# Optimization experiments

Hardware: AMD Instinct MI355X
Metric: run time of the kernel (lower is better)

The kernel has to match this reference:

```python
import jax, jax.numpy as jnp
import numpy as np

N_NODES = 100000

def setup_inputs() -> dict:
    key = jax.random.key(0)
    k1, k2, k3, k4, k5 = jax.random.split(key, 5)
    F_in, H, C = 128, 64, 40
    x = jax.random.normal(k1, (N_NODES, F_in), dtype=jnp.float32)
    edge_index = jax.random.randint(k2, (2, 1600000), 0, N_NODES, dtype=jnp.int64)
    # GCNConv weights (no bias), Glorot-ish scale
    W0 = jax.random.normal(k3, (F_in, H), dtype=jnp.float32) / np.sqrt(F_in)
    W1 = jax.random.normal(k4, (H, H), dtype=jnp.float32) / np.sqrt(H)
    W2 = jax.random.normal(k5, (H, C), dtype=jnp.float32) / np.sqrt(H)
    return {"x": x, "edge_index": edge_index, "W0": W0, "W1": W1, "W2": W2}


def _gcn_norm(edge_index, num_nodes):
    # Add self-loops, compute symmetric normalization D^-1/2 A D^-1/2
    loop = jnp.arange(num_nodes, dtype=edge_index.dtype)
    src = jnp.concatenate([edge_index[0], loop])
    dst = jnp.concatenate([edge_index[1], loop])
    deg = jax.ops.segment_sum(jnp.ones_like(dst, dtype=jnp.float32), dst,
                              num_segments=num_nodes)
    dinv = jnp.where(deg > 0, jax.lax.rsqrt(deg), 0.0)
    norm = dinv[src] * dinv[dst]  # [E + N]
    return src, dst, norm


def reference(x, edge_index, W0, W1, W2):
    N = x.shape[0]
    src, dst, norm = _gcn_norm(edge_index, N)

    def conv(h, W):
        h = h @ W                                   # [N, d_out]
        msg = h[src] * norm[:, None]                # gather + scale  [E+N, d_out]
        return jax.ops.segment_sum(msg, dst, num_segments=N)

    h = jax.nn.relu(conv(x, W0))
    h = jax.nn.relu(conv(h, W1))
    h = jax.nn.relu(conv(h, W2))
    return h
```

## Files before the change

### kernel.cpp

```cpp
#include <hip/hip_runtime.h>
#include <hip/hip_fp16.h>

#define N_FEAT0 128
#define HID 64
#define NCLS 40

#define BSH 9
#define BSZ 512
#define BCAP 12288
#define STILE 16384

__global__ __launch_bounds__(256) void scatter_kernel(const int* __restrict__ esrc,
                                                      const int* __restrict__ edst,
                                                      int* __restrict__ bfill,
                                                      int* __restrict__ slab, int E) {
  __shared__ int cnt[256];
  __shared__ int base[256];
  int t = threadIdx.x;
  int t0 = blockIdx.x * STILE;
  cnt[t] = 0;
  __syncthreads();

#pragma unroll 4
  for (int i = 0; i < STILE / 1024; ++i) {
    int e = t0 + i * 1024 + t * 4;
    if (e < E) {
      int4 d4 = *(const int4*)(edst + e);
      atomicAdd(&cnt[d4.x >> BSH], 1);
      atomicAdd(&cnt[d4.y >> BSH], 1);
      atomicAdd(&cnt[d4.z >> BSH], 1);
      atomicAdd(&cnt[d4.w >> BSH], 1);
    }
  }
  __syncthreads();
  int c = cnt[t];
  if (c > 0) base[t] = t * BCAP + atomicAdd(&bfill[t], c);
  cnt[t] = 0;
  __syncthreads();

#pragma unroll 4
  for (int i = 0; i < STILE / 1024; ++i) {
    int e = t0 + i * 1024 + t * 4;
    if (e < E) {
      int4 s4 = *(const int4*)(esrc + e);
      int4 d4 = *(const int4*)(edst + e);
#define EMIT(dd, ss)                                             \
      {                                                          \
        int b_ = (dd) >> BSH;                                    \
        int r_ = atomicAdd(&cnt[b_], 1);                         \
        slab[base[b_] + r_] = (((dd) & (BSZ - 1)) << 17) | (ss); \
      }
      EMIT(d4.x, s4.x)
      EMIT(d4.y, s4.y)
      EMIT(d4.z, s4.z)
      EMIT(d4.w, s4.w)
#undef EMIT
    }
  }
}

__global__ __launch_bounds__(256) void build_kernel(const int* __restrict__ slab,
                                                    const int* __restrict__ bfill,
                                                    int* __restrict__ row_ptr,
                                                    float* __restrict__ dinv,
                                                    int* __restrict__ ew,
                                                    int N, int nbuck) {
  __shared__ int cnt[512];
  __shared__ int pre[512];
  __shared__ int s2[256];
  int b = blockIdx.x;
  int t = threadIdx.x;
  int nbase = b << BSH;
  int nNodes = N - nbase;
  if (nNodes > BSZ) nNodes = BSZ;

  s2[t] = (t < nbuck) ? bfill[t] : 0;
  __syncthreads();
  for (int off = 1; off < 256; off <<= 1) {
    int u = (t >= off) ? s2[t - off] : 0;
    __syncthreads();
    s2[t] += u;
    __syncthreads();
  }
  int sz = bfill[b];
  int obase = s2[b] - sz;
  if (b == 0 && t == 255) row_ptr[N] = s2[255];
  __syncthreads();

  cnt[t] = 0;
  cnt[t + 256] = 0;
  __syncthreads();

  int sbeg = b * BCAP;

  for (int r = t; r < sz; r += 256) atomicAdd(&cnt[((unsigned)slab[sbeg + r]) >> 17], 1);
  __syncthreads();

  int a = cnt[2 * t], c = cnt[2 * t + 1];
  s2[t] = a + c;
  __syncthreads();
  for (int off = 1; off < 256; off <<= 1) {
    int u = (t >= off) ? s2[t - off] : 0;
    __syncthreads();
    s2[t] += u;
    __syncthreads();
  }
  int ex = s2[t] - (a + c);
  pre[2 * t] = ex;
  pre[2 * t + 1] = ex + a;
  __syncthreads();

  if (t < nNodes) {
    row_ptr[nbase + t] = obase + pre[t];
    dinv[nbase + t] = rsqrtf((float)(cnt[t] + 1));
  }
  int t2 = t + 256;
  if (t2 < nNodes) {
    row_ptr[nbase + t2] = obase + pre[t2];
    dinv[nbase + t2] = rsqrtf((float)(cnt[t2] + 1));
  }
  __syncthreads();
  cnt[t] = 0;
  cnt[t + 256] = 0;
  __syncthreads();

  for (int r = t; r < sz; r += 256) {
    int rec = slab[sbeg + r];
    int dloc = ((unsigned)rec) >> 17;
    int rank = atomicAdd(&cnt[dloc], 1);
    ew[obase + pre[dloc] + rank] = rec & 0x1FFFF;
  }
}

template <int K, int NC>
__global__ __launch_bounds__(256) void gemm_kernel(const float* __restrict__ A,
                                                   const float* __restrict__ W,
                                                   __half* __restrict__ Out,
                                                   const float* __restrict__ rowscale,
                                                   int N) {
  constexpr int BK = 64;
  constexpr int LDSS = 68;
  __shared__ float As[128 * LDSS];

  int t = threadIdx.x;
  int lane = t & 63;
  int wave = t >> 6;
  int c4 = lane & 15;
  int qr = lane >> 4;
  int r0 = blockIdx.x * 128;

  int wc = 4 * c4;
  if (wc > NC - 4) wc = NC - 4;
  bool cok = (wc == 4 * c4);

  float4 acc[8];
#pragma unroll
  for (int m = 0; m < 8; ++m) acc[m] = make_float4(0.f, 0.f, 0.f, 0.f);

  for (int kc = 0; kc < K; kc += BK) {
    __syncthreads();
#pragma unroll
    for (int i = 0; i < 8; ++i) {
      int idx = t + i * 256;
      int row = idx >> 4;
      int cq = idx & 15;
      int gr = r0 + row;
      if (gr >= N) gr = N - 1;
      float4 v = *(const float4*)(A + (size_t)gr * K + kc + 4 * cq);
      *(float4*)(As + row * LDSS + 4 * cq) = v;
    }
    __syncthreads();

#pragma unroll 2
    for (int kk = 0; kk < BK / 4; ++kk) {
      float4 w[4];
#pragma unroll
      for (int k = 0; k < 4; ++k)
        w[k] = *(const float4*)(W + (size_t)(kc + kk * 4 + k) * NC + wc);
#pragma unroll
      for (int m = 0; m < 8; ++m) {
        int lrow = wave * 32 + qr + 4 * m;
        float4 a = *(const float4*)(As + lrow * LDSS + kk * 4);
        acc[m].x = fmaf(a.x, w[0].x, acc[m].x);
        acc[m].y = fmaf(a.x, w[0].y, acc[m].y);
        acc[m].z = fmaf(a.x, w[0].z, acc[m].z);
        acc[m].w = fmaf(a.x, w[0].w, acc[m].w);
        acc[m].x = fmaf(a.y, w[1].x, acc[m].x);
        acc[m].y = fmaf(a.y, w[1].y, acc[m].y);
        acc[m].z = fmaf(a.y, w[1].z, acc[m].z);
        acc[m].w = fmaf(a.y, w[1].w, acc[m].w);
        acc[m].x = fmaf(a.z, w[2].x, acc[m].x);
        acc[m].y = fmaf(a.z, w[2].y, acc[m].y);
        acc[m].z = fmaf(a.z, w[2].z, acc[m].z);
        acc[m].w = fmaf(a.z, w[2].w, acc[m].w);
        acc[m].x = fmaf(a.w, w[3].x, acc[m].x);
        acc[m].y = fmaf(a.w, w[3].y, acc[m].y);
        acc[m].z = fmaf(a.w, w[3].z, acc[m].z);
        acc[m].w = fmaf(a.w, w[3].w, acc[m].w);
      }
    }
  }

  if (cok) {
#pragma unroll
    for (int m = 0; m < 8; ++m) {
      int gr = r0 + wave * 32 + qr + 4 * m;
      if (gr < N) {
        float ds = rowscale[gr];
        union { __half2 h[2]; uint2 u; } cv;
        cv.h[0] = __floats2half2_rn(ds * acc[m].x, ds * acc[m].y);
        cv.h[1] = __floats2half2_rn(ds * acc[m].z, ds * acc[m].w);
        *(uint2*)(Out + (size_t)gr * NC + wc) = cv.u;
      }
    }
  }
}

template <int NC>
__global__ __launch_bounds__(256) void gemm_h_kernel(const __half* __restrict__ A,
                                                     const float* __restrict__ W,
                                                     __half* __restrict__ Out,
                                                     const float* __restrict__ rowscale,
                                                     int N) {
  constexpr int K = 64;
  constexpr int LDSH = 76;
  __shared__ __half As[128 * LDSH];

  int t = threadIdx.x;
  int lane = t & 63;
  int wave = t >> 6;
  int c4 = lane & 15;
  int qr = lane >> 4;
  int r0 = blockIdx.x * 128;

  int wc = 4 * c4;
  if (wc > NC - 4) wc = NC - 4;
  bool cok = (wc == 4 * c4);

  float4 acc[8];
#pragma unroll
  for (int m = 0; m < 8; ++m) acc[m] = make_float4(0.f, 0.f, 0.f, 0.f);

#pragma unroll
  for (int i = 0; i < 4; ++i) {
    int idx = t + i * 256;
    int row = idx >> 3;
    int cq = idx & 7;
    int gr = r0 + row;
    if (gr >= N) gr = N - 1;
    uint4 v = *(const uint4*)(A + (size_t)gr * K + cq * 8);
    *(uint4*)(As + row * LDSH + cq * 8) = v;
  }
  __syncthreads();

#pragma unroll 2
  for (int kk = 0; kk < 8; ++kk) {
    float4 w[8];
#pragma unroll
    for (int k = 0; k < 8; ++k)
      w[k] = *(const float4*)(W + (size_t)(kk * 8 + k) * NC + wc);
#pragma unroll
    for (int m = 0; m < 8; ++m) {
      int lrow = wave * 32 + qr + 4 * m;
      uint4 av = *(const uint4*)(As + lrow * LDSH + kk * 8);
      const __half2* h2 = (const __half2*)&av;
      float2 f0 = __half22float2(h2[0]);
      float2 f1 = __half22float2(h2[1]);
      float2 f2 = __half22float2(h2[2]);
      float2 f3 = __half22float2(h2[3]);
#define FMA4(aa, ww)                              \
      acc[m].x = fmaf(aa, ww.x, acc[m].x);        \
      acc[m].y = fmaf(aa, ww.y, acc[m].y);        \
      acc[m].z = fmaf(aa, ww.z, acc[m].z);        \
      acc[m].w = fmaf(aa, ww.w, acc[m].w);
      FMA4(f0.x, w[0]) FMA4(f0.y, w[1])
      FMA4(f1.x, w[2]) FMA4(f1.y, w[3])
      FMA4(f2.x, w[4]) FMA4(f2.y, w[5])
      FMA4(f3.x, w[6]) FMA4(f3.y, w[7])
#undef FMA4
    }
  }

  if (cok) {
#pragma unroll
    for (int m = 0; m < 8; ++m) {
      int gr = r0 + wave * 32 + qr + 4 * m;
      if (gr < N) {
        float ds = rowscale[gr];
        union { __half2 h[2]; uint2 u; } cv;
        cv.h[0] = __floats2half2_rn(ds * acc[m].x, ds * acc[m].y);
        cv.h[1] = __floats2half2_rn(ds * acc[m].z, ds * acc[m].w);
        *(uint2*)(Out + (size_t)gr * NC + wc) = cv.u;
      }
    }
  }
}

template <int F, bool HOUT>
__global__ __launch_bounds__(256) void agg_kernel(const __half* __restrict__ G,
                                                  const int* __restrict__ row_ptr,
                                                  const int* __restrict__ ew,
                                                  const float* __restrict__ dinv,
                                                  void* __restrict__ HoutV, int N) {
  constexpr int FO = F / 8;
  int gid = blockIdx.x * blockDim.x + threadIdx.x;
  int v = gid >> 6;
  if (v >= N) return;
  int lane = threadIdx.x & 63;
  int eg = lane >> 3;
  int fo = lane & 7;
  bool fok = (fo < FO);
  int foc = fok ? fo : FO - 1;

  float acc[8];
#pragma unroll
  for (int i = 0; i < 8; ++i) acc[i] = 0.f;

#define GLD(s) (*(const uint4*)(G + (size_t)(s) * F + foc * 8))
  auto addrow = [&](uint4 q) {
    const __half2* h = (const __half2*)&q;
#pragma unroll
    for (int i = 0; i < 4; ++i) {
      float2 f = __half22float2(h[i]);
      acc[2 * i] += f.x;
      acc[2 * i + 1] += f.y;
    }
  };

  if (eg == 0) addrow(GLD(v));

  int beg = __builtin_amdgcn_readfirstlane(row_ptr[v]);
  int end = __builtin_amdgcn_readfirstlane(row_ptr[v + 1]);
  int j = beg;
  for (; j + 16 <= end; j += 16) {
    int s0 = ew[j + eg];
    int s1 = ew[j + 8 + eg];
    uint4 a = GLD(s0);
    uint4 b = GLD(s1);
    addrow(a);
    addrow(b);
  }
  if (j + 8 <= end) {
    addrow(GLD(ew[j + eg]));
    j += 8;
  }
  {
    int idx = j + eg;
    if (idx < end) addrow(GLD(ew[idx]));
  }
#undef GLD

#pragma unroll
  for (int m = 8; m <= 32; m <<= 1) {
#pragma unroll
    for (int i = 0; i < 8; ++i) acc[i] += __shfl_xor(acc[i], m);
  }

  if (fok) {
    float dv = dinv[v];
    if constexpr (HOUT) {
      __half* Hout = (__half*)HoutV;
      union { __half2 h2[4]; uint4 u; } cv;
      cv.h2[0] = __floats2half2_rn(fmaxf(dv * acc[0], 0.f), fmaxf(dv * acc[1], 0.f));
      cv.h2[1] = __floats2half2_rn(fmaxf(dv * acc[2], 0.f), fmaxf(dv * acc[3], 0.f));
      cv.h2[2] = __floats2half2_rn(fmaxf(dv * acc[4], 0.f), fmaxf(dv * acc[5], 0.f));
      cv.h2[3] = __floats2half2_rn(fmaxf(dv * acc[6], 0.f), fmaxf(dv * acc[7], 0.f));
      *(uint4*)(Hout + (size_t)v * F + fo * 8) = cv.u;
    } else {
      float* Hout = (float*)HoutV;
      float4 o0, o1;
      o0.x = fmaxf(dv * acc[0], 0.f);
      o0.y = fmaxf(dv * acc[1], 0.f);
      o0.z = fmaxf(dv * acc[2], 0.f);
      o0.w = fmaxf(dv * acc[3], 0.f);
      o1.x = fmaxf(dv * acc[4], 0.f);
      o1.y = fmaxf(dv * acc[5], 0.f);
      o1.z = fmaxf(dv * acc[6], 0.f);
      o1.w = fmaxf(dv * acc[7], 0.f);
      float4* outp = (float4*)(Hout + (size_t)v * F + fo * 8);
      outp[0] = o0;
      outp[1] = o1;
    }
  }
}

extern "C" void kernel_launch(void* const* d_in, const int* in_sizes, int n_in,
                              void* d_out, int out_size, void* d_ws, size_t ws_size,
                              hipStream_t stream) {
  const float* x  = (const float*)d_in[0];
  const int*   eg = (const int*)d_in[1];
  const float* W0 = (const float*)d_in[2];
  const float* W1 = (const float*)d_in[3];
  const float* W2 = (const float*)d_in[4];
  float* out = (float*)d_out;

  const int N = in_sizes[0] / N_FEAT0;
  const int E = in_sizes[1] / 2;
  const int* esrc = eg;
  const int* edst = eg + E;
  const int nbuck = (N + BSZ - 1) >> BSH;

  char* p = (char*)d_ws;
  auto alloc = [&](size_t bytes) {
    char* r = p;
    p += (bytes + 255) & ~(size_t)255;
    return r;
  };
  int*    bfill   = (int*)alloc(256 * 4);
  int*    row_ptr = (int*)alloc((size_t)(N + 1) * 4);
  float*  dinv    = (float*)alloc((size_t)N * 4);
  int*    ew      = (int*)alloc((size_t)E * 4);
  __half* bufG    = (__half*)alloc((size_t)N * HID * 2);
  __half* bufH    = (__half*)alloc((size_t)N * HID * 2);
  __half* bufG3   = (__half*)alloc((size_t)N * NCLS * 2);
  int* slab = (int*)bufH;

  hipMemsetAsync(bfill, 0, 256 * 4, stream);

  const int sblocks = (E + STILE - 1) / STILE;
  scatter_kernel<<<sblocks, 256, 0, stream>>>(esrc, edst, bfill, slab, E);
  build_kernel<<<nbuck, 256, 0, stream>>>(slab, bfill, row_ptr, dinv, ew, N, nbuck);

  const int gblocks = (N + 127) / 128;
  const int ablocks = (N + 3) / 4;
  gemm_kernel<128, 64><<<gblocks, 256, 0, stream>>>(x, W0, bufG, dinv, N);
  agg_kernel<64, true><<<ablocks, 256, 0, stream>>>(bufG, row_ptr, ew, dinv, bufH, N);
  gemm_h_kernel<64><<<gblocks, 256, 0, stream>>>(bufH, W1, bufG, dinv, N);
  agg_kernel<64, true><<<ablocks, 256, 0, stream>>>(bufG, row_ptr, ew, dinv, bufH, N);
  gemm_h_kernel<40><<<gblocks, 256, 0, stream>>>(bufH, W2, bufG3, dinv, N);
  agg_kernel<40, false><<<ablocks, 256, 0, stream>>>(bufG3, row_ptr, ew, dinv, out, N);
}
```

Measured before the change: 346.3 us.

## Store hidden features in feature-planar layout and aggregate one plane per block

The GEMM kernels now write the 64-wide hidden features as eight planes of 8 halves per node instead of row-major. A new aggregation kernel assigns each block to one feature plane and a chunk of nodes, with 16 lanes per node walking the neighbour list. The aim is to shrink the gathered working set per plane (N*16 bytes) so random neighbour gathers hit in cache better. In exchange the CSR row_ptr and edge list are read eight times, each gather is only 16 bytes, and a fixed grid of 2048 blocks is used.

```diff
diff --git a/kernel.cpp b/kernel.cpp
--- a/kernel.cpp
+++ b/kernel.cpp
@@ -150,8 +150,6 @@
   int r0 = blockIdx.x * 128;
 
   int wc = 4 * c4;
-  if (wc > NC - 4) wc = NC - 4;
-  bool cok = (wc == 4 * c4);
 
   float4 acc[8];
 #pragma unroll
@@ -201,7 +199,9 @@
     }
   }
 
-  if (cok) {
+  {
+    int plane = c4 >> 1;
+    int hoff = (c4 & 1) * 4;
 #pragma unroll
     for (int m = 0; m < 8; ++m) {
       int gr = r0 + wave * 32 + qr + 4 * m;
@@ -210,13 +210,13 @@
         union { __half2 h[2]; uint2 u; } cv;
         cv.h[0] = __floats2half2_rn(ds * acc[m].x, ds * acc[m].y);
         cv.h[1] = __floats2half2_rn(ds * acc[m].z, ds * acc[m].w);
-        *(uint2*)(Out + (size_t)gr * NC + wc) = cv.u;
+        *(uint2*)(Out + (size_t)plane * N * 8 + (size_t)gr * 8 + hoff) = cv.u;
       }
     }
   }
 }
 
-template <int NC>
+template <int NC, bool PLANAR>
 __global__ __launch_bounds__(256) void gemm_h_kernel(const __half* __restrict__ A,
                                                      const float* __restrict__ W,
                                                      __half* __restrict__ Out,
@@ -290,18 +290,82 @@
         union { __half2 h[2]; uint2 u; } cv;
         cv.h[0] = __floats2half2_rn(ds * acc[m].x, ds * acc[m].y);
         cv.h[1] = __floats2half2_rn(ds * acc[m].z, ds * acc[m].w);
-        *(uint2*)(Out + (size_t)gr * NC + wc) = cv.u;
+        if constexpr (PLANAR) {
+          int plane = c4 >> 1;
+          int hoff = (c4 & 1) * 4;
+          *(uint2*)(Out + (size_t)plane * N * 8 + (size_t)gr * 8 + hoff) = cv.u;
+        } else {
+          *(uint2*)(Out + (size_t)gr * NC + wc) = cv.u;
+        }
       }
     }
   }
 }
 
-template <int F, bool HOUT>
+__global__ __launch_bounds__(256) void aggs_kernel(const __half* __restrict__ Gp,
+                                                   const int* __restrict__ row_ptr,
+                                                   const int* __restrict__ ew,
+                                                   const float* __restrict__ dinv,
+                                                   __half* __restrict__ Hout, int N) {
+  int fo = blockIdx.x & 7;
+  int chunk = blockIdx.x >> 3;
+  int nch = gridDim.x >> 3;
+  int lane = threadIdx.x & 63;
+  int wv = threadIdx.x >> 6;
+  int grp = lane >> 4;
+  int lig = lane & 15;
+  const __half* g = Gp + (size_t)fo * N * 8;
+
+  int per = (N + nch - 1) / nch;
+  int v0 = chunk * per;
+  int v1 = v0 + per;
+  if (v1 > N) v1 = N;
+
+  for (int v = v0 + wv * 4 + grp; v < v1; v += 16) {
+    float acc[8];
+#pragma unroll
+    for (int i = 0; i < 8; ++i) acc[i] = 0.f;
+
+#define GLD(s) (*(const uint4*)(g + (size_t)(s) * 8))
+    auto addrow = [&](uint4 q) {
+      const __half2* h2 = (const __half2*)&q;
+#pragma unroll
+      for (int i = 0; i < 4; ++i) {
+        float2 f2 = __half22float2(h2[i]);
+        acc[2 * i] += f2.x;
+        acc[2 * i + 1] += f2.y;
+      }
+    };
+
+    int beg = row_ptr[v];
+    int end = row_ptr[v + 1];
+    if (lig == 0) addrow(GLD(v));
+    for (int j = beg + lig; j < end; j += 16) addrow(GLD(ew[j]));
+#undef GLD
+
+#pragma unroll
+    for (int m = 1; m <= 8; m <<= 1)
+#pragma unroll
+      for (int i = 0; i < 8; ++i) acc[i] += __shfl_xor(acc[i], m);
+
+    if (lig == 0) {
+      float dv = dinv[v];
+      union { __half2 h2[4]; uint4 u; } cv;
+      cv.h2[0] = __floats2half2_rn(fmaxf(dv * acc[0], 0.f), fmaxf(dv * acc[1], 0.f));
+      cv.h2[1] = __floats2half2_rn(fmaxf(dv * acc[2], 0.f), fmaxf(dv * acc[3], 0.f));
+      cv.h2[2] = __floats2half2_rn(fmaxf(dv * acc[4], 0.f), fmaxf(dv * acc[5], 0.f));
+      cv.h2[3] = __floats2half2_rn(fmaxf(dv * acc[6], 0.f), fmaxf(dv * acc[7], 0.f));
+      *(uint4*)(Hout + (size_t)v * HID + fo * 8) = cv.u;
+    }
+  }
+}
+
+template <int F>
 __global__ __launch_bounds__(256) void agg_kernel(const __half* __restrict__ G,
                                                   const int* __restrict__ row_ptr,
                                                   const int* __restrict__ ew,
                                                   const float* __restrict__ dinv,
-                                                  void* __restrict__ HoutV, int N) {
+                                                  float* __restrict__ Hout, int N) {
   constexpr int FO = F / 8;
   int gid = blockIdx.x * blockDim.x + threadIdx.x;
   int v = gid >> 6;
@@ -358,29 +422,18 @@
 
   if (fok) {
     float dv = dinv[v];
-    if constexpr (HOUT) {
-      __half* Hout = (__half*)HoutV;
-      union { __half2 h2[4]; uint4 u; } cv;
-      cv.h2[0] = __floats2half2_rn(fmaxf(dv * acc[0], 0.f), fmaxf(dv * acc[1], 0.f));
-      cv.h2[1] = __floats2half2_rn(fmaxf(dv * acc[2], 0.f), fmaxf(dv * acc[3], 0.f));
-      cv.h2[2] = __floats2half2_rn(fmaxf(dv * acc[4], 0.f), fmaxf(dv * acc[5], 0.f));
-      cv.h2[3] = __floats2half2_rn(fmaxf(dv * acc[6], 0.f), fmaxf(dv * acc[7], 0.f));
-      *(uint4*)(Hout + (size_t)v * F + fo * 8) = cv.u;
-    } else {
-      float* Hout = (float*)HoutV;
-      float4 o0, o1;
-      o0.x = fmaxf(dv * acc[0], 0.f);
-      o0.y = fmaxf(dv * acc[1], 0.f);
-      o0.z = fmaxf(dv * acc[2], 0.f);
-      o0.w = fmaxf(dv * acc[3], 0.f);
-      o1.x = fmaxf(dv * acc[4], 0.f);
-      o1.y = fmaxf(dv * acc[5], 0.f);
-      o1.z = fmaxf(dv * acc[6], 0.f);
-      o1.w = fmaxf(dv * acc[7], 0.f);
-      float4* outp = (float4*)(Hout + (size_t)v * F + fo * 8);
-      outp[0] = o0;
-      outp[1] = o1;
-    }
+    float4 o0, o1;
+    o0.x = fmaxf(dv * acc[0], 0.f);
+    o0.y = fmaxf(dv * acc[1], 0.f);
+    o0.z = fmaxf(dv * acc[2], 0.f);
+    o0.w = fmaxf(dv * acc[3], 0.f);
+    o1.x = fmaxf(dv * acc[4], 0.f);
+    o1.y = fmaxf(dv * acc[5], 0.f);
+    o1.z = fmaxf(dv * acc[6], 0.f);
+    o1.w = fmaxf(dv * acc[7], 0.f);
+    float4* outp = (float4*)(Hout + (size_t)v * F + fo * 8);
+    outp[0] = o0;
+    outp[1] = o1;
   }
 }
 
@@ -423,10 +476,11 @@
 
   const int gblocks = (N + 127) / 128;
   const int ablocks = (N + 3) / 4;
+  const int sgrid = 8 * 256;
   gemm_kernel<128, 64><<<gblocks, 256, 0, stream>>>(x, W0, bufG, dinv, N);
-  agg_kernel<64, true><<<ablocks, 256, 0, stream>>>(bufG, row_ptr, ew, dinv, bufH, N);
-  gemm_h_kernel<64><<<gblocks, 256, 0, stream>>>(bufH, W1, bufG, dinv, N);
-  agg_kernel<64, true><<<ablocks, 256, 0, stream>>>(bufG, row_ptr, ew, dinv, bufH, N);
-  gemm_h_kernel<40><<<gblocks, 256, 0, stream>>>(bufH, W2, bufG3, dinv, N);
-  agg_kernel<40, false><<<ablocks, 256, 0, stream>>>(bufG3, row_ptr, ew, dinv, out, N);
-}
+  aggs_kernel<<<sgrid, 256, 0, stream>>>(bufG, row_ptr, ew, dinv, bufH, N);
+  gemm_h_kernel<64, true><<<gblocks, 256, 0, stream>>>(bufH, W1, bufG, dinv, N);
+  aggs_kernel<<<sgrid, 256, 0, stream>>>(bufG, row_ptr, ew, dinv, bufH, N);
+  gemm_h_kernel<40, false><<<gblocks, 256, 0, stream>>>(bufH, W2, bufG3, dinv, N);
+  agg_kernel<40><<<ablocks, 256, 0, stream>>>(bufG3, row_ptr, ew, dinv, out, N);
+}
```

Result: slower. 429.7 us (+24.1%).
